# Performance work log

Hardware: AMD Instinct MI355X
Metric: run time of the kernel (lower is better)

The kernel has to match this reference:

```python
import jax, jax.numpy as jnp
import numpy as np

D = 128        # dim
S = 64         # seq_len
NSYM = 128     # symbols
STACK = 16     # stack_size
DEPTH = 8      # max_depth (ACT recursion)
THRESH = 0.99  # act_threshold
EPS = 1e-6
RES = 0.1      # residual_weight
LAM_E = 0.01   # lambda_energy
TEMP = 1.0
B = 512


def _clin(xr, xi, Wr, Wi):
    # ComplexLinear: (Wr + i Wi)(xr + i xi)
    return xr @ Wr.T - xi @ Wi.T, xr @ Wi.T + xi @ Wr.T


def _cattn(zr, zi, wr, wi):
    # ComplexAttention: complex QKV projections, real softmax over concat(real,imag)
    qr, qi = _clin(zr, zi, wr[0], wi[0])
    kr, ki = _clin(zr, zi, wr[1], wi[1])
    vr, vi = _clin(zr, zi, wr[2], wi[2])
    qf = jnp.concatenate([qr, qi], -1)
    kf = jnp.concatenate([kr, ki], -1)
    a = jax.nn.softmax(jnp.einsum('bsd,btd->bst', qf, kf) * (D ** -0.5), axis=-1)
    return jnp.einsum('bst,btd->bsd', a, vr), jnp.einsum('bst,btd->bsd', a, vi)


def setup_inputs() -> dict:
    key = jax.random.key(0)
    ks = jax.random.split(key, 12)
    sc = 1.0 / np.sqrt(D)
    return {
        'z_real': jax.random.normal(ks[0], (B, S, D), jnp.float32),
        'z_imag': jax.random.normal(ks[1], (B, S, D), jnp.float32),
        'attn_wr': jax.random.normal(ks[2], (3, D, D), jnp.float32) * sc,
        'attn_wi': jax.random.normal(ks[3], (3, D, D), jnp.float32) * sc,
        'mem_wr': jax.random.normal(ks[4], (3, D, D), jnp.float32) * sc,
        'mem_wi': jax.random.normal(ks[5], (3, D, D), jnp.float32) * sc,
        'ctrl_w': jax.random.normal(ks[6], (2 * D, 3), jnp.float32) * sc,
        'ctrl_b': jnp.zeros((3,), jnp.float32),
        'halt_w': jax.random.normal(ks[7], (2 * D, 1), jnp.float32) * sc,
        'halt_b': jnp.zeros((1,), jnp.float32),
        'codebook': jax.random.normal(ks[8], (NSYM, 2 * D), jnp.float32) * 0.2,
        'adjacency': jax.random.normal(ks[9], (NSYM, NSYM), jnp.float32),
    }


def reference(z_real, z_imag, attn_wr, attn_wi, mem_wr, mem_wi,
              ctrl_w, ctrl_b, halt_w, halt_b, codebook, adjacency):
    b = z_real.shape[0]
    mem0 = jnp.zeros((b, STACK, 2 * D), z_real.dtype)
    ptr0 = jnp.zeros((b, STACK), z_real.dtype).at[:, 0].set(1.0)
    probs0 = jnp.zeros((b, NSYM), z_real.dtype)
    halt0 = jnp.zeros((b,), z_real.dtype)
    acc0 = jnp.zeros((b, S, 2 * D), z_real.dtype)

    def step(carry, t):
        zr, zi, mem, ptr, prev_probs, halt_acc, acc = carry
        # --- complex self-attention with residual recursion ---
        ar, ai = _cattn(zr, zi, attn_wr, attn_wi)
        zr = ar + RES * zr
        zi = ai + RES * zi
        # --- memory stack (push/pop/stay pointer machine) ---
        zf = jnp.concatenate([zr.mean(1), zi.mean(1)], -1)  # [B, 2D]
        g = jax.nn.sigmoid(zf @ ctrl_w + ctrl_b)
        tot = g.sum(-1, keepdims=True) + EPS
        push, pop, stay = g[:, 0:1] / tot, g[:, 1:2] / tot, g[:, 2:3] / tot
        ptr = push * jnp.roll(ptr, 1, axis=1) + pop * jnp.roll(ptr, -1, axis=1) + stay * ptr
        mem = mem * (1 - push[..., None]) + push[..., None] * zf[:, None, :]
        amr, ami = _cattn(mem[..., :D], mem[..., D:], mem_wr, mem_wi)
        read = (jnp.concatenate([amr, ami], -1) * ptr[..., None]).sum(1)  # [B, 2D]
        zr = zr + RES * read[:, None, :D]
        zi = zi + RES * read[:, None, D:]
        # --- grounded graph VQ: codebook distance + adjacency energy bias ---
        zf = jnp.concatenate([zr.mean(1), zi.mean(1)], -1)
        d = ((zf ** 2).sum(-1, keepdims=True) + (codebook ** 2).sum(-1)
             - 2 * zf @ codebook.T) / (2 * D)
        mag = jnp.sqrt(zr ** 2 + zi ** 2)
        up = jax.nn.softplus(mag.var() / (1.0 + EPS))  # complexity modulation
        gb = prev_probs @ adjacency
        d_tot = jnp.where(t == 0, d, d - LAM_E * up * jax.nn.sigmoid(gb))
        probs = jax.nn.softmax(-d_tot / TEMP, axis=-1)
        quant = probs @ codebook
        zr = zr + RES * quant[:, None, :D]
        zi = zi + RES * quant[:, None, D:]
        # --- ACT halting accumulation ---
        p = jax.nn.sigmoid(zf @ halt_w + halt_b)[:, 0]
        running = (halt_acc < THRESH).astype(zr.dtype)
        w = jnp.where(halt_acc + p * running >= THRESH, 1.0 - halt_acc, p) * running
        halt_acc = halt_acc + w
        acc = acc + w[:, None, None] * jnp.concatenate([zr, zi], -1)
        return (zr, zi, mem, ptr, probs, halt_acc, acc), None

    carry, _ = jax.lax.scan(step, (z_real, z_imag, mem0, ptr0, probs0, halt0, acc0),
                            jnp.arange(DEPTH))
    return carry[6]  # ACT-weighted state, [B, S, 2D]
```

## Files before the change

kernel.cpp:

```cpp
#include <hip/hip_runtime.h>
#include <math.h>

#define BB 512
#define SS 64
#define DD 128
#define FF 256
#define NSYM 128
#define STK 16
#define NDEPTH 8

typedef _Float16 half_t;
typedef __attribute__((ext_vector_type(4))) _Float16 half4;
typedef __attribute__((ext_vector_type(8))) _Float16 half8;
typedef __attribute__((ext_vector_type(4))) float f32x4;

#define Z_OFF      0ull
#define QKV_OFF    8388608ull
#define WVM_OFF    33554432ull
#define MV_OFF     35651584ull
#define SIG_OFF    35782656ull
#define ZF1_OFF    41951232ull
#define ZF2_OFF    42082304ull
#define READ_OFF   42213376ull
#define PROBS_OFF  42344448ull
#define DELTA_OFF  42409984ull
#define HALT_OFF   42541056ull
#define PVAL_OFF   42541568ull
#define WACT_OFF   42542080ull
#define MAGP_OFF   42542592ull
#define CB2_OFF    42936832ull

__global__ void k_buildwt32(const float* __restrict__ wr, const float* __restrict__ wi,
                            float* __restrict__ WT32) {
    int idx = blockIdx.x * 256 + threadIdx.x;
    if (idx >= 768 * 256) return;
    int col = idx >> 8;
    int e   = idx & 255;
    int h   = col >> 8;
    int c   = col & 255;
    const float* Wr = wr + h * DD * DD;
    const float* Wi = wi + h * DD * DD;
    float v;
    if (c < DD) {
        v = (e < DD) ? Wr[c * DD + e] : -Wi[c * DD + (e - DD)];
    } else {
        int j = c - DD;
        v = (e < DD) ? Wi[j * DD + e] : Wr[j * DD + (e - DD)];
    }
    WT32[idx] = v;
}

__global__ __launch_bounds__(256) void k_buildG(const float* __restrict__ WT32,
                                                half_t* __restrict__ GTh,
                                                half_t* __restrict__ GTl) {
    __shared__ float kcol[256];
    int n = blockIdx.x;
    int e = threadIdx.x;
    kcol[e] = WT32[65536 + e * 256 + n];
    __syncthreads();
    float s = 0.f;
    for (int c = 0; c < 256; ++c) s += kcol[c] * WT32[c * 256 + e];
    half_t h = (half_t)s;
    GTh[n * 256 + e] = h;
    GTl[n * 256 + e] = (half_t)(s - (float)h);
}

__global__ void k_splitWv(const float* __restrict__ WT32,
                          half_t* __restrict__ WvTh, half_t* __restrict__ WvTl) {
    int idx = blockIdx.x * 256 + threadIdx.x;
    float v = WT32[131072 + idx];
    half_t h = (half_t)v;
    WvTh[idx] = h;
    WvTl[idx] = (half_t)(v - (float)h);
}

__global__ void k_buildWv32m(const float* __restrict__ wr, const float* __restrict__ wi,
                             float* __restrict__ Wv32m) {
    int idx = blockIdx.x * 256 + threadIdx.x;
    int e = idx >> 8;
    int c = idx & 255;
    const float* Wr = wr + 2 * DD * DD;
    const float* Wi = wi + 2 * DD * DD;
    float v;
    if (c < DD) {
        v = (e < DD) ? Wr[c * DD + e] : -Wi[c * DD + (e - DD)];
    } else {
        int j = c - DD;
        v = (e < DD) ? Wi[j * DD + e] : Wr[j * DD + (e - DD)];
    }
    Wv32m[idx] = v;
}

__global__ void k_cb2(const float* __restrict__ cb, float* __restrict__ cb2) {
    int n = threadIdx.x;
    float s = 0.f;
    for (int c = 0; c < FF; ++c) { float v = cb[n * FF + c]; s += v * v; }
    cb2[n] = s;
}

__global__ __launch_bounds__(256) void k_init(const float* __restrict__ zr_in,
                                              const float* __restrict__ zi_in,
                                              float* __restrict__ z, float* __restrict__ mv,
                                              float* __restrict__ sigma,
                                              float* __restrict__ halt, float* __restrict__ acc,
                                              float* __restrict__ delta, float* __restrict__ wact) {
    size_t idx = (size_t)blockIdx.x * 256 + threadIdx.x;
    int c = (int)(idx & 255);
    size_t bs = idx >> 8;
    z[idx] = (c < DD) ? zr_in[bs * DD + c] : zi_in[bs * DD + (c - DD)];
    acc[idx] = 0.f;
    if (idx < 131072) { mv[idx] = 0.f; delta[idx] = 0.f; }
    if (idx < 512)   { halt[idx] = 0.f; wact[idx] = 0.f; sigma[idx] = 1.f; }
}

__global__ __launch_bounds__(512, 1) void k_attn8(
        float* __restrict__ z,
        const half_t* __restrict__ GTh, const half_t* __restrict__ GTl,
        const half_t* __restrict__ WvTh, const half_t* __restrict__ WvTl,
        const float* __restrict__ delta, const float* __restrict__ wact,
        float* __restrict__ acc, float* __restrict__ zf1g) {
    __shared__ half_t Zh[16896];
    __shared__ half_t Zl[16896];
    __shared__ half_t Ubuf[2][18432];
    __shared__ half_t Pbuf[2][4][1152];
    __shared__ float Smx[4][2][16];
    __shared__ float Ssum[4][2][16];

    int b = blockIdx.x, tid = threadIdx.x;
    int w = tid >> 6, lane = tid & 63;
    int l15 = lane & 15, lq = lane >> 4;
    float* zb = z + (size_t)b * (SS * FF);
    float* accb = acc + (size_t)b * (SS * FF);

    float wa = wact[b];
    f32x4 dv = *(const f32x4*)(delta + b * FF + lane * 4);
    bool doacc = (wa != 0.0f);
#pragma unroll
    for (int it = 0; it < 8; ++it) {
        int i = w * 8 + it;
        f32x4 zv = *(const f32x4*)(zb + (size_t)i * FF + lane * 4);
        f32x4 x0;
#pragma unroll
        for (int jj = 0; jj < 4; ++jj) x0[jj] = zv[jj] + 0.1f * dv[jj];
        if (doacc) {
            f32x4 av = *(const f32x4*)(accb + (size_t)i * FF + lane * 4);
#pragma unroll
            for (int jj = 0; jj < 4; ++jj) av[jj] += wa * x0[jj];
            *(f32x4*)(accb + (size_t)i * FF + lane * 4) = av;
        }
        half4 h4, l4;
#pragma unroll
        for (int jj = 0; jj < 4; ++jj) {
            half_t h = (half_t)x0[jj];
            h4[jj] = h; l4[jj] = (half_t)(x0[jj] - (float)h);
        }
        *(half4*)&Zh[i * 264 + lane * 4] = h4;
        *(half4*)&Zl[i * 264 + lane * 4] = l4;
    }
    __syncthreads();

    {
        f32x4 tac[4][2];
#pragma unroll
        for (int mt = 0; mt < 4; ++mt)
#pragma unroll
            for (int nt = 0; nt < 2; ++nt) tac[mt][nt] = (f32x4){0.f, 0.f, 0.f, 0.f};
        __builtin_amdgcn_s_setprio(1);
#pragma unroll 2
        for (int kt = 0; kt < 8; ++kt) {
            int kc = kt * 32 + lq * 8;
            half8 ah[4], al[4], gh[2], gl[2];
#pragma unroll
            for (int mt = 0; mt < 4; ++mt) {
                int ro = (mt * 16 + l15) * 264 + kc;
                ah[mt] = *(const half8*)&Zh[ro];
                al[mt] = *(const half8*)&Zl[ro];
            }
#pragma unroll
            for (int nt = 0; nt < 2; ++nt) {
                size_t go = (size_t)(w * 32 + nt * 16 + l15) * 256 + kc;
                gh[nt] = *(const half8*)(GTh + go);
                gl[nt] = *(const half8*)(GTl + go);
            }
#pragma unroll
            for (int mt = 0; mt < 4; ++mt)
#pragma unroll
                for (int nt = 0; nt < 2; ++nt) {
                    tac[mt][nt] = __builtin_amdgcn_mfma_f32_16x16x32_f16(ah[mt], gh[nt], tac[mt][nt], 0, 0, 0);
                    tac[mt][nt] = __builtin_amdgcn_mfma_f32_16x16x32_f16(ah[mt], gl[nt], tac[mt][nt], 0, 0, 0);
                    tac[mt][nt] = __builtin_amdgcn_mfma_f32_16x16x32_f16(al[mt], gh[nt], tac[mt][nt], 0, 0, 0);
                }
        }
        __builtin_amdgcn_s_setprio(0);
        const float scale = 0.08838834764831845f;
#pragma unroll
        for (int mt = 0; mt < 4; ++mt)
#pragma unroll
            for (int nt = 0; nt < 2; ++nt)
#pragma unroll
                for (int r = 0; r < 4; ++r) {
                    int m = mt * 16 + lq * 4 + r;
                    int n = w * 32 + nt * 16 + l15;
                    float v = tac[mt][nt][r] * scale;
                    half_t h = (half_t)v;
                    Ubuf[0][m * 264 + n] = h;
                    Ubuf[1][m * 264 + n] = (half_t)(v - (float)h);
                }
    }
    __syncthreads();

    int qb = w & 3;
    int jh = w >> 2;
    float sv[2][4];
    {
        f32x4 sac[2];
        sac[0] = (f32x4){0.f, 0.f, 0.f, 0.f};
        sac[1] = (f32x4){0.f, 0.f, 0.f, 0.f};
        __builtin_amdgcn_s_setprio(1);
#pragma unroll 2
        for (int kt = 0; kt < 8; ++kt) {
            int kc = kt * 32 + lq * 8;
            int to = (qb * 16 + l15) * 264 + kc;
            half8 bh = *(const half8*)&Ubuf[0][to];
            half8 bl = *(const half8*)&Ubuf[1][to];
            half8 ah[2], al[2];
#pragma unroll
            for (int jt = 0; jt < 2; ++jt) {
                int ro = ((jh * 2 + jt) * 16 + l15) * 264 + kc;
                ah[jt] = *(const half8*)&Zh[ro];
                al[jt] = *(const half8*)&Zl[ro];
            }
#pragma unroll
            for (int jt = 0; jt < 2; ++jt) {
                sac[jt] = __builtin_amdgcn_mfma_f32_16x16x32_f16(ah[jt], bh, sac[jt], 0, 0, 0);
                sac[jt] = __builtin_amdgcn_mfma_f32_16x16x32_f16(ah[jt], bl, sac[jt], 0, 0, 0);
                sac[jt] = __builtin_amdgcn_mfma_f32_16x16x32_f16(al[jt], bh, sac[jt], 0, 0, 0);
            }
        }
        __builtin_amdgcn_s_setprio(0);
        float mxh = -1e30f;
#pragma unroll
        for (int jt = 0; jt < 2; ++jt)
#pragma unroll
            for (int r = 0; r < 4; ++r) { sv[jt][r] = sac[jt][r]; mxh = fmaxf(mxh, sv[jt][r]); }
        mxh = fmaxf(mxh, __shfl_xor(mxh, 16));
        mxh = fmaxf(mxh, __shfl_xor(mxh, 32));
        float sumh = 0.f;
#pragma unroll
        for (int jt = 0; jt < 2; ++jt)
#pragma unroll
            for (int r = 0; r < 4; ++r) { float e = expf(sv[jt][r] - mxh); sv[jt][r] = e; sumh += e; }
        sumh += __shfl_xor(sumh, 16);
        sumh += __shfl_xor(sumh, 32);
        if (lq == 0) { Smx[qb][jh][l15] = mxh; Ssum[qb][jh][l15] = sumh; }
    }

    f32x4 vac[4][2];
#pragma unroll
    for (int mt = 0; mt < 4; ++mt)
#pragma unroll
        for (int nt = 0; nt < 2; ++nt) vac[mt][nt] = (f32x4){0.f, 0.f, 0.f, 0.f};
    __builtin_amdgcn_s_setprio(1);
#pragma unroll 2
    for (int kt = 0; kt < 8; ++kt) {
        int kc = kt * 32 + lq * 8;
        half8 ah[4], al[4], gh[2], gl[2];
#pragma unroll
        for (int mt = 0; mt < 4; ++mt) {
            int ro = (mt * 16 + l15) * 264 + kc;
            ah[mt] = *(const half8*)&Zh[ro];
            al[mt] = *(const half8*)&Zl[ro];
        }
#pragma unroll
        for (int nt = 0; nt < 2; ++nt) {
            size_t go = (size_t)(w * 32 + nt * 16 + l15) * 256 + kc;
            gh[nt] = *(const half8*)(WvTh + go);
            gl[nt] = *(const half8*)(WvTl + go);
        }
#pragma unroll
        for (int mt = 0; mt < 4; ++mt)
#pragma unroll
            for (int nt = 0; nt < 2; ++nt) {
                vac[mt][nt] = __builtin_amdgcn_mfma_f32_16x16x32_f16(ah[mt], gh[nt], vac[mt][nt], 0, 0, 0);
                vac[mt][nt] = __builtin_amdgcn_mfma_f32_16x16x32_f16(ah[mt], gl[nt], vac[mt][nt], 0, 0, 0);
                vac[mt][nt] = __builtin_amdgcn_mfma_f32_16x16x32_f16(al[mt], gh[nt], vac[mt][nt], 0, 0, 0);
            }
    }
    __builtin_amdgcn_s_setprio(0);
    __syncthreads();

    {
        float mx0 = Smx[qb][0][l15], mx1 = Smx[qb][1][l15];
        float gmx = fmaxf(mx0, mx1);
        float ssum = Ssum[qb][0][l15] * expf(mx0 - gmx) + Ssum[qb][1][l15] * expf(mx1 - gmx);
        float pscale = expf(((jh == 0) ? mx0 : mx1) - gmx) / ssum;
#pragma unroll
        for (int jt = 0; jt < 2; ++jt) {
            half4 h4, l4;
#pragma unroll
            for (int r = 0; r < 4; ++r) {
                float pv = sv[jt][r] * pscale;
                half_t hh = (half_t)pv;
                h4[r] = hh;
                l4[r] = (half_t)(pv - (float)hh);
            }
            int po = l15 * 72 + (jh * 2 + jt) * 16 + lq * 4;
            *(half4*)&Pbuf[0][qb][po] = h4;
            *(half4*)&Pbuf[1][qb][po] = l4;
        }
    }

#pragma unroll
    for (int mt = 0; mt < 4; ++mt)
#pragma unroll
        for (int nt = 0; nt < 2; ++nt) {
            int n = w * 32 + nt * 16 + l15;
            int m0 = mt * 16 + lq * 4;
            half4 h4, l4;
#pragma unroll
            for (int r = 0; r < 4; ++r) {
                float v = vac[mt][nt][r];
                half_t h = (half_t)v;
                h4[r] = h; l4[r] = (half_t)(v - (float)h);
            }
            *(half4*)&Ubuf[0][n * 72 + m0] = h4;
            *(half4*)&Ubuf[1][n * 72 + m0] = l4;
        }
    __syncthreads();

    f32x4 oc[4][2];
#pragma unroll
    for (int mt = 0; mt < 4; ++mt)
#pragma unroll
        for (int nt = 0; nt < 2; ++nt) oc[mt][nt] = (f32x4){0.f, 0.f, 0.f, 0.f};
    __builtin_amdgcn_s_setprio(1);
#pragma unroll
    for (int kt = 0; kt < 2; ++kt) {
        half8 pah[4], pal[4];
#pragma unroll
        for (int mt = 0; mt < 4; ++mt) {
            int po = l15 * 72 + kt * 32 + lq * 8;
            pah[mt] = *(const half8*)&Pbuf[0][mt][po];
            pal[mt] = *(const half8*)&Pbuf[1][mt][po];
        }
#pragma unroll
        for (int nt = 0; nt < 2; ++nt) {
            int n = w * 32 + nt * 16 + l15;
            half8 vbh = *(const half8*)&Ubuf[0][n * 72 + kt * 32 + lq * 8];
            half8 vbl = *(const half8*)&Ubuf[1][n * 72 + kt * 32 + lq * 8];
#pragma unroll
            for (int mt = 0; mt < 4; ++mt) {
                oc[mt][nt] = __builtin_amdgcn_mfma_f32_16x16x32_f16(pah[mt], vbh, oc[mt][nt], 0, 0, 0);
                oc[mt][nt] = __builtin_amdgcn_mfma_f32_16x16x32_f16(pah[mt], vbl, oc[mt][nt], 0, 0, 0);
                oc[mt][nt] = __builtin_amdgcn_mfma_f32_16x16x32_f16(pal[mt], vbh, oc[mt][nt], 0, 0, 0);
            }
        }
    }
    __builtin_amdgcn_s_setprio(0);

    float zfs[2] = {0.f, 0.f};
#pragma unroll
    for (int mt = 0; mt < 4; ++mt)
#pragma unroll
        for (int nt = 0; nt < 2; ++nt)
#pragma unroll
            for (int r = 0; r < 4; ++r) {
                int i = mt * 16 + lq * 4 + r;
                int c = w * 32 + nt * 16 + l15;
                int zo = i * 264 + c;
                float x0 = (float)Zh[zo] + (float)Zl[zo];
                float z1 = oc[mt][nt][r] + 0.1f * x0;
                zb[(size_t)i * FF + c] = z1;
                zfs[nt] += z1;
            }
#pragma unroll
    for (int nt = 0; nt < 2; ++nt) {
        zfs[nt] += __shfl_xor(zfs[nt], 16);
        zfs[nt] += __shfl_xor(zfs[nt], 32);
    }
    if (lq == 0) {
#pragma unroll
        for (int nt = 0; nt < 2; ++nt)
            zf1g[b * FF + w * 32 + nt * 16 + l15] = zfs[nt] * (1.f / 64.f);
    }
}

__global__ __launch_bounds__(256) void k_stack3(
        const float* __restrict__ zf1,
        const float* __restrict__ ctrl_w, const float* __restrict__ ctrl_b,
        float* __restrict__ sigma, float* __restrict__ mv,
        const float* __restrict__ Wv32m,
        float* __restrict__ readv, float* __restrict__ zf2,
        const float* __restrict__ halt_w, const float* __restrict__ halt_b,
        float* __restrict__ pval,
        const float* __restrict__ z, float* __restrict__ magpart) {
    __shared__ float zf[256];
    __shared__ float g[3];
    __shared__ float rd[256];
    __shared__ float red[256];

    int b = blockIdx.x, tid = threadIdx.x;
    int w = tid >> 6, lane = tid & 63;

    zf[tid] = zf1[b * FF + tid];
    __syncthreads();

    float zw = 0.f;
#pragma unroll 8
    for (int e = 0; e < 256; ++e) zw += Wv32m[e * 256 + tid] * zf[e];

    if (w < 3) {
        float s = 0.f;
#pragma unroll
        for (int q = 0; q < 4; ++q) {
            int c = lane + 64 * q;
            s += zf[c] * ctrl_w[c * 3 + w];
        }
#pragma unroll
        for (int off = 1; off < 64; off <<= 1) s += __shfl_xor(s, off);
        if (lane == 0) g[w] = 1.f / (1.f + expf(-(s + ctrl_b[w])));
    }
    __syncthreads();
    float tot = g[0] + g[1] + g[2] + 1e-6f;
    float push = g[0] / tot, pop = g[1] / tot, stay = g[2] / tot;
    float signew = sigma[b] * (push + pop + stay);
    if (tid == 0) sigma[b] = signew;

    float omp = 1.f - push;
    float m2v = mv[b * FF + tid] * omp + push * zw;
    mv[b * FF + tid] = m2v;

    float a = signew * m2v;
    rd[tid] = a;
    readv[b * FF + tid] = a;
    float z2 = zf[tid] + 0.1f * a;
    zf2[b * FF + tid] = z2;
    red[tid] = z2 * halt_w[tid];
    __syncthreads();
    for (int off = 128; off > 0; off >>= 1) {
        if (tid < off) red[tid] += red[tid + off];
        __syncthreads();
    }
    if (tid == 0) pval[b] = 1.f / (1.f + expf(-(red[0] + halt_b[0])));
    __syncthreads();

    {
        int d = tid & 127, hf = tid >> 7;
        float rr = 0.1f * rd[d];
        float ri = 0.1f * rd[DD + d];
        const float* zb = z + (size_t)b * (SS * FF);
        float ms = 0.f, msq = 0.f;
        for (int s32 = 0; s32 < 32; ++s32) {
            int s = hf * 32 + s32;
            float zr = zb[s * FF + d] + rr;
            float zi = zb[s * FF + DD + d] + ri;
            float m2 = zr * zr + zi * zi;
            ms += sqrtf(m2); msq += m2;
        }
        red[tid] = ms;
        __syncthreads();
        for (int off = 128; off > 0; off >>= 1) {
            if (tid < off) red[tid] += red[tid + off];
            __syncthreads();
        }
        float tms = red[0];
        __syncthreads();
        red[tid] = msq;
        __syncthreads();
        for (int off = 128; off > 0; off >>= 1) {
            if (tid < off) red[tid] += red[tid + off];
            __syncthreads();
        }
        if (tid == 0) { magpart[2 * b] = tms; magpart[2 * b + 1] = red[0]; }
    }
}

__global__ __launch_bounds__(256) void k_vq2(
        const float* __restrict__ zf2g, const float* __restrict__ readv,
        float* __restrict__ probs, float* __restrict__ halt,
        const float* __restrict__ pvalg, const float* __restrict__ magp,
        const float* __restrict__ cb, const float* __restrict__ cb2,
        const float* __restrict__ adj,
        float* __restrict__ delta, float* __restrict__ wact,
        const float* __restrict__ z, float* __restrict__ acc,
        int t, int last) {
    __shared__ float zf[256];
    __shared__ float pr[128];
    __shared__ float upred[8];
    __shared__ float zzred[4];
    __shared__ float mxred[4];
    __shared__ float sered[4];
    __shared__ float waS[1];

    int b = blockIdx.x, tid = threadIdx.x;
    int w = tid >> 6, lane = tid & 63;

    zf[tid] = zf2g[b * FF + tid];

    float up = 0.f;
    if (t > 0) {
        f32x4 mv4 = *(const f32x4*)(magp + tid * 4);
        float pa = mv4[0] + mv4[2];
        float pb = mv4[1] + mv4[3];
#pragma unroll
        for (int off = 1; off < 64; off <<= 1) {
            pa += __shfl_xor(pa, off);
            pb += __shfl_xor(pb, off);
        }
        if (lane == 0) { upred[w * 2] = pa; upred[w * 2 + 1] = pb; }
    }
    __syncthreads();
    if (t > 0) {
        float tms  = upred[0] + upred[2] + upred[4] + upred[6];
        float tmsq = upred[1] + upred[3] + upred[5] + upred[7];
        const float N = 4194304.f;
        float mean = tms / N;
        float var = tmsq / N - mean * mean;
        float x = var / (1.f + 1e-6f);
        up = (x > 20.f) ? x : log1pf(expf(x));
    }

    {
        float part = zf[tid] * zf[tid];
#pragma unroll
        for (int off = 1; off < 64; off <<= 1) part += __shfl_xor(part, off);
        if (lane == 0) zzred[w] = part;
    }
    __syncthreads();
    float zz = zzred[0] + zzred[1] + zzred[2] + zzred[3];

    int n = tid >> 1, half = tid & 1;
    float dacc = 0.f;
    {
        const float* cbn = cb + n * FF + half * 128;
        const float* zfp = zf + half * 128;
#pragma unroll 8
        for (int c2 = 0; c2 < 128; c2 += 4) {
            f32x4 cv = *(const f32x4*)(cbn + c2);
            dacc += cv[0] * zfp[c2] + cv[1] * zfp[c2 + 1] + cv[2] * zfp[c2 + 2] + cv[3] * zfp[c2 + 3];
        }
        dacc += __shfl_xor(dacc, 1);
    }
    float gacc = 0.f;
    if (t > 0) {
        const float* pp = probs + b * NSYM;
        for (int k = half * 64; k < half * 64 + 64; ++k)
            gacc += pp[k] * adj[k * NSYM + n];
        gacc += __shfl_xor(gacc, 1);
    }

    float dist = (zz + cb2[n] - 2.f * dacc) * (1.f / 256.f);
    float dtot = dist;
    if (t > 0) dtot = dist - 0.01f * up * (1.f / (1.f + expf(-gacc)));
    float vval = -dtot;

    {
        float m = vval;
#pragma unroll
        for (int off = 1; off < 64; off <<= 1) m = fmaxf(m, __shfl_xor(m, off));
        if (lane == 0) mxred[w] = m;
    }
    __syncthreads();
    float mx = fmaxf(fmaxf(mxred[0], mxred[1]), fmaxf(mxred[2], mxred[3]));

    float e = expf(vval - mx);
    {
        float s = (half == 0) ? e : 0.f;
#pragma unroll
        for (int off = 1; off < 64; off <<= 1) s += __shfl_xor(s, off);
        if (lane == 0) sered[w] = s;
    }
    __syncthreads();
    float se = sered[0] + sered[1] + sered[2] + sered[3];
    float psm = e / se;
    if (half == 0) {
        pr[n] = psm;
        probs[b * NSYM + n] = psm;
    }
    __syncthreads();

    float q = 0.f;
#pragma unroll 4
    for (int k = 0; k < NSYM; ++k) q += pr[k] * cb[k * FF + tid];
    float dltc = readv[b * FF + tid] + q;
    delta[b * FF + tid] = dltc;

    if (tid == 0) {
        float h = halt[b], p = pvalg[b];
        float running = (h < 0.99f) ? 1.f : 0.f;
        float w2 = (((h + p * running) >= 0.99f) ? (1.f - h) : p) * running;
        halt[b] = h + w2;
        wact[b] = w2;
        waS[0] = w2;
    }

    if (last) {
        __syncthreads();
        float wa = waS[0];
        if (wa != 0.0f) {
            const float* zb = z + (size_t)b * (SS * FF);
            float* ab = acc + (size_t)b * (SS * FF);
            for (int s = 0; s < SS; ++s)
                ab[s * FF + tid] += wa * (zb[s * FF + tid] + 0.1f * dltc);
        }
    }
}

extern "C" void kernel_launch(void* const* d_in, const int* in_sizes, int n_in,
                              void* d_out, int out_size, void* d_ws, size_t ws_size,
                              hipStream_t stream) {
    const float* z_real  = (const float*)d_in[0];
    const float* z_imag  = (const float*)d_in[1];
    const float* attn_wr = (const float*)d_in[2];
    const float* attn_wi = (const float*)d_in[3];
    const float* mem_wr  = (const float*)d_in[4];
    const float* mem_wi  = (const float*)d_in[5];
    const float* ctrl_w  = (const float*)d_in[6];
    const float* ctrl_b  = (const float*)d_in[7];
    const float* halt_w  = (const float*)d_in[8];
    const float* halt_b  = (const float*)d_in[9];
    const float* codebook  = (const float*)d_in[10];
    const float* adjacency = (const float*)d_in[11];

    float* ws = (float*)d_ws;
    float* z      = ws + Z_OFF;
    float* WT32   = ws + QKV_OFF;
    half_t* GTh   = (half_t*)(ws + QKV_OFF + 196608);
    half_t* GTl   = GTh + 65536;
    half_t* WvTh  = GTl + 65536;
    half_t* WvTl  = WvTh + 65536;
    float* Wv32m  = ws + WVM_OFF;
    float* mv     = ws + MV_OFF;
    float* sigma  = ws + SIG_OFF;
    float* zf1    = ws + ZF1_OFF;
    float* zf2    = ws + ZF2_OFF;
    float* readv  = ws + READ_OFF;
    float* probs  = ws + PROBS_OFF;
    float* delta  = ws + DELTA_OFF;
    float* halt   = ws + HALT_OFF;
    float* pval   = ws + PVAL_OFF;
    float* wact   = ws + WACT_OFF;
    float* magp   = ws + MAGP_OFF;
    float* cb2    = ws + CB2_OFF;
    float* acc    = (float*)d_out;

    k_buildwt32<<<768, 256, 0, stream>>>(attn_wr, attn_wi, WT32);
    k_buildG<<<256, 256, 0, stream>>>(WT32, GTh, GTl);
    k_splitWv<<<256, 256, 0, stream>>>(WT32, WvTh, WvTl);
    k_buildWv32m<<<256, 256, 0, stream>>>(mem_wr, mem_wi, Wv32m);
    k_cb2<<<1, 128, 0, stream>>>(codebook, cb2);
    k_init<<<32768, 256, 0, stream>>>(z_real, z_imag, z, mv, sigma, halt, acc,
                                      delta, wact);

    for (int t = 0; t < NDEPTH; ++t) {
        k_attn8<<<BB, 512, 0, stream>>>(z, GTh, GTl, WvTh, WvTl, delta, wact, acc, zf1);
        k_stack3<<<BB, 256, 0, stream>>>(zf1, ctrl_w, ctrl_b, sigma, mv, Wv32m,
                                         readv, zf2, halt_w, halt_b, pval, z, magp);
        k_vq2<<<BB, 256, 0, stream>>>(zf2, readv, probs, halt, pval, magp,
                                      codebook, cb2, adjacency, delta, wact,
                                      z, acc, t, (t == NDEPTH - 1) ? 1 : 0);
    }
}
```

Measured before the change: 781.7 us.

## Fuse stack-memory update and magnitude statistics into attention kernel

Merges the k_stack3 kernel into k_attn8 so the per-batch mean vector, stack controller, memory-read, halting logit and magnitude partial sums are computed in the same block that produced z. The new z tile is kept in shared memory (reusing the Zh/Zl region as fp32) so the magnitude pass reads from LDS instead of re-reading z from global memory. Tree reductions are replaced with wave shuffles. This removes one kernel launch per depth step and a global round trip of z, at the cost of a larger shared-memory footprint and more work per attention block.

```diff
diff --git a/kernel.cpp b/kernel.cpp
--- a/kernel.cpp
+++ b/kernel.cpp
@@ -19,7 +19,6 @@
 #define WVM_OFF    33554432ull
 #define MV_OFF     35651584ull
 #define SIG_OFF    35782656ull
-#define ZF1_OFF    41951232ull
 #define ZF2_OFF    42082304ull
 #define READ_OFF   42213376ull
 #define PROBS_OFF  42344448ull
@@ -118,19 +117,35 @@
         const half_t* __restrict__ GTh, const half_t* __restrict__ GTl,
         const half_t* __restrict__ WvTh, const half_t* __restrict__ WvTl,
         const float* __restrict__ delta, const float* __restrict__ wact,
-        float* __restrict__ acc, float* __restrict__ zf1g) {
-    __shared__ half_t Zh[16896];
-    __shared__ half_t Zl[16896];
-    __shared__ half_t Ubuf[2][18432];
-    __shared__ half_t Pbuf[2][4][1152];
-    __shared__ float Smx[4][2][16];
-    __shared__ float Ssum[4][2][16];
+        float* __restrict__ acc,
+        const float* __restrict__ Wv32m,
+        const float* __restrict__ ctrl_w, const float* __restrict__ ctrl_b,
+        const float* __restrict__ halt_w, const float* __restrict__ halt_b,
+        float* __restrict__ sigma, float* __restrict__ mv,
+        float* __restrict__ readv, float* __restrict__ zf2,
+        float* __restrict__ pval, float* __restrict__ magpart) {
+    __shared__ __align__(16) char smem[160768];
+    half_t* Zh = (half_t*)smem;
+    half_t* Zl = (half_t*)(smem + 33792);
+    float*  Zf = (float*)smem;
+    half_t* U0 = (half_t*)(smem + 67584);
+    half_t* U1 = (half_t*)(smem + 104448);
+    half_t* P0 = (half_t*)(smem + 141312);
+    half_t* P1 = (half_t*)(smem + 150528);
+    float* Smx = (float*)(smem + 159744);
+    float* Ssu = (float*)(smem + 160256);
+    float* zfS = (float*)(smem + 67584);
+    float* zwS = (float*)(smem + 68608);
+    float* rdS = (float*)(smem + 69632);
+    float* redS= (float*)(smem + 70656);
+    float* gS  = (float*)(smem + 71680);
 
     int b = blockIdx.x, tid = threadIdx.x;
     int w = tid >> 6, lane = tid & 63;
     int l15 = lane & 15, lq = lane >> 4;
     float* zb = z + (size_t)b * (SS * FF);
     float* accb = acc + (size_t)b * (SS * FF);
+    float sigold = sigma[b];
 
     float wa = wact[b];
     f32x4 dv = *(const f32x4*)(delta + b * FF + lane * 4);
@@ -203,8 +218,8 @@
                     int n = w * 32 + nt * 16 + l15;
                     float v = tac[mt][nt][r] * scale;
                     half_t h = (half_t)v;
-                    Ubuf[0][m * 264 + n] = h;
-                    Ubuf[1][m * 264 + n] = (half_t)(v - (float)h);
+                    U0[m * 264 + n] = h;
+                    U1[m * 264 + n] = (half_t)(v - (float)h);
                 }
     }
     __syncthreads();
@@ -221,8 +236,8 @@
         for (int kt = 0; kt < 8; ++kt) {
             int kc = kt * 32 + lq * 8;
             int to = (qb * 16 + l15) * 264 + kc;
-            half8 bh = *(const half8*)&Ubuf[0][to];
-            half8 bl = *(const half8*)&Ubuf[1][to];
+            half8 bh = *(const half8*)&U0[to];
+            half8 bl = *(const half8*)&U1[to];
             half8 ah[2], al[2];
 #pragma unroll
             for (int jt = 0; jt < 2; ++jt) {
@@ -252,7 +267,7 @@
             for (int r = 0; r < 4; ++r) { float e = expf(sv[jt][r] - mxh); sv[jt][r] = e; sumh += e; }
         sumh += __shfl_xor(sumh, 16);
         sumh += __shfl_xor(sumh, 32);
-        if (lq == 0) { Smx[qb][jh][l15] = mxh; Ssum[qb][jh][l15] = sumh; }
+        if (lq == 0) { Smx[(qb * 2 + jh) * 16 + l15] = mxh; Ssu[(qb * 2 + jh) * 16 + l15] = sumh; }
     }
 
     f32x4 vac[4][2];
@@ -290,9 +305,10 @@
     __syncthreads();
 
     {
-        float mx0 = Smx[qb][0][l15], mx1 = Smx[qb][1][l15];
+        float mx0 = Smx[(qb * 2 + 0) * 16 + l15], mx1 = Smx[(qb * 2 + 1) * 16 + l15];
         float gmx = fmaxf(mx0, mx1);
-        float ssum = Ssum[qb][0][l15] * expf(mx0 - gmx) + Ssum[qb][1][l15] * expf(mx1 - gmx);
+        float ssum = Ssu[(qb * 2 + 0) * 16 + l15] * expf(mx0 - gmx)
+                   + Ssu[(qb * 2 + 1) * 16 + l15] * expf(mx1 - gmx);
         float pscale = expf(((jh == 0) ? mx0 : mx1) - gmx) / ssum;
 #pragma unroll
         for (int jt = 0; jt < 2; ++jt) {
@@ -305,8 +321,8 @@
                 l4[r] = (half_t)(pv - (float)hh);
             }
             int po = l15 * 72 + (jh * 2 + jt) * 16 + lq * 4;
-            *(half4*)&Pbuf[0][qb][po] = h4;
-            *(half4*)&Pbuf[1][qb][po] = l4;
+            *(half4*)&P0[qb * 1152 + po] = h4;
+            *(half4*)&P1[qb * 1152 + po] = l4;
         }
     }
 
@@ -323,8 +339,8 @@
                 half_t h = (half_t)v;
                 h4[r] = h; l4[r] = (half_t)(v - (float)h);
             }
-            *(half4*)&Ubuf[0][n * 72 + m0] = h4;
-            *(half4*)&Ubuf[1][n * 72 + m0] = l4;
+            *(half4*)&U0[n * 72 + m0] = h4;
+            *(half4*)&U1[n * 72 + m0] = l4;
         }
     __syncthreads();
 
@@ -340,14 +356,14 @@
 #pragma unroll
         for (int mt = 0; mt < 4; ++mt) {
             int po = l15 * 72 + kt * 32 + lq * 8;
-            pah[mt] = *(const half8*)&Pbuf[0][mt][po];
-            pal[mt] = *(const half8*)&Pbuf[1][mt][po];
+            pah[mt] = *(const half8*)&P0[mt * 1152 + po];
+            pal[mt] = *(const half8*)&P1[mt * 1152 + po];
         }
 #pragma unroll
         for (int nt = 0; nt < 2; ++nt) {
             int n = w * 32 + nt * 16 + l15;
-            half8 vbh = *(const half8*)&Ubuf[0][n * 72 + kt * 32 + lq * 8];
-            half8 vbl = *(const half8*)&Ubuf[1][n * 72 + kt * 32 + lq * 8];
+            half8 vbh = *(const half8*)&U0[n * 72 + kt * 32 + lq * 8];
+            half8 vbl = *(const half8*)&U1[n * 72 + kt * 32 + lq * 8];
 #pragma unroll
             for (int mt = 0; mt < 4; ++mt) {
                 oc[mt][nt] = __builtin_amdgcn_mfma_f32_16x16x32_f16(pah[mt], vbh, oc[mt][nt], 0, 0, 0);
@@ -370,6 +386,7 @@
                 int zo = i * 264 + c;
                 float x0 = (float)Zh[zo] + (float)Zl[zo];
                 float z1 = oc[mt][nt][r] + 0.1f * x0;
+                oc[mt][nt][r] = z1;
                 zb[(size_t)i * FF + c] = z1;
                 zfs[nt] += z1;
             }
@@ -378,100 +395,98 @@
         zfs[nt] += __shfl_xor(zfs[nt], 16);
         zfs[nt] += __shfl_xor(zfs[nt], 32);
     }
+    __syncthreads();
+
+#pragma unroll
+    for (int mt = 0; mt < 4; ++mt)
+#pragma unroll
+        for (int nt = 0; nt < 2; ++nt)
+#pragma unroll
+            for (int r = 0; r < 4; ++r) {
+                int i = mt * 16 + lq * 4 + r;
+                int c = w * 32 + nt * 16 + l15;
+                Zf[i * 256 + c] = oc[mt][nt][r];
+            }
     if (lq == 0) {
 #pragma unroll
         for (int nt = 0; nt < 2; ++nt)
-            zf1g[b * FF + w * 32 + nt * 16 + l15] = zfs[nt] * (1.f / 64.f);
-    }
-}
-
-__global__ __launch_bounds__(256) void k_stack3(
-        const float* __restrict__ zf1,
-        const float* __restrict__ ctrl_w, const float* __restrict__ ctrl_b,
-        float* __restrict__ sigma, float* __restrict__ mv,
-        const float* __restrict__ Wv32m,
-        float* __restrict__ readv, float* __restrict__ zf2,
-        const float* __restrict__ halt_w, const float* __restrict__ halt_b,
-        float* __restrict__ pval,
-        const float* __restrict__ z, float* __restrict__ magpart) {
-    __shared__ float zf[256];
-    __shared__ float g[3];
-    __shared__ float rd[256];
-    __shared__ float red[256];
-
-    int b = blockIdx.x, tid = threadIdx.x;
-    int w = tid >> 6, lane = tid & 63;
-
-    zf[tid] = zf1[b * FF + tid];
-    __syncthreads();
-
-    float zw = 0.f;
-#pragma unroll 8
-    for (int e = 0; e < 256; ++e) zw += Wv32m[e * 256 + tid] * zf[e];
+            zfS[w * 32 + nt * 16 + l15] = zfs[nt] * (1.f / 64.f);
+    }
+    __syncthreads();
 
     if (w < 3) {
         float s = 0.f;
 #pragma unroll
         for (int q = 0; q < 4; ++q) {
             int c = lane + 64 * q;
-            s += zf[c] * ctrl_w[c * 3 + w];
+            s += zfS[c] * ctrl_w[c * 3 + w];
         }
 #pragma unroll
         for (int off = 1; off < 64; off <<= 1) s += __shfl_xor(s, off);
-        if (lane == 0) g[w] = 1.f / (1.f + expf(-(s + ctrl_b[w])));
-    }
-    __syncthreads();
-    float tot = g[0] + g[1] + g[2] + 1e-6f;
-    float push = g[0] / tot, pop = g[1] / tot, stay = g[2] / tot;
-    float signew = sigma[b] * (push + pop + stay);
-    if (tid == 0) sigma[b] = signew;
-
-    float omp = 1.f - push;
-    float m2v = mv[b * FF + tid] * omp + push * zw;
-    mv[b * FF + tid] = m2v;
-
-    float a = signew * m2v;
-    rd[tid] = a;
-    readv[b * FF + tid] = a;
-    float z2 = zf[tid] + 0.1f * a;
-    zf2[b * FF + tid] = z2;
-    red[tid] = z2 * halt_w[tid];
-    __syncthreads();
-    for (int off = 128; off > 0; off >>= 1) {
-        if (tid < off) red[tid] += red[tid + off];
-        __syncthreads();
-    }
-    if (tid == 0) pval[b] = 1.f / (1.f + expf(-(red[0] + halt_b[0])));
-    __syncthreads();
-
-    {
-        int d = tid & 127, hf = tid >> 7;
-        float rr = 0.1f * rd[d];
-        float ri = 0.1f * rd[DD + d];
-        const float* zb = z + (size_t)b * (SS * FF);
+        if (lane == 0) gS[w] = 1.f / (1.f + expf(-(s + ctrl_b[w])));
+    } else if (w >= 4) {
+        int c = (w - 4) * 64 + lane;
+        float s = 0.f;
+#pragma unroll 8
+        for (int e = 0; e < 256; ++e) s += Wv32m[e * 256 + c] * zfS[e];
+        zwS[c] = s;
+    }
+    __syncthreads();
+
+    float z2 = 0.f;
+    {
+        float tot = gS[0] + gS[1] + gS[2] + 1e-6f;
+        float push = gS[0] / tot, pop = gS[1] / tot, stay = gS[2] / tot;
+        float signew = sigold * (push + pop + stay);
+        if (tid == 0) sigma[b] = signew;
+        if (tid < 256) {
+            float m2v = mv[b * FF + tid] * (1.f - push) + push * zwS[tid];
+            mv[b * FF + tid] = m2v;
+            float a = signew * m2v;
+            rdS[tid] = a;
+            readv[b * FF + tid] = a;
+            z2 = zfS[tid] + 0.1f * a;
+            zf2[b * FF + tid] = z2;
+        }
+    }
+    {
+        float hp = (tid < 256) ? z2 * halt_w[tid] : 0.f;
+#pragma unroll
+        for (int off = 1; off < 64; off <<= 1) hp += __shfl_xor(hp, off);
+        if (lane == 0) redS[w] = hp;
+    }
+    __syncthreads();
+    if (tid == 0) {
+        float s = redS[0] + redS[1] + redS[2] + redS[3] + redS[4] + redS[5] + redS[6] + redS[7];
+        pval[b] = 1.f / (1.f + expf(-(s + halt_b[0])));
+    }
+
+    {
+        int d = tid & 127, seg = tid >> 7;
+        float rr = 0.1f * rdS[d];
+        float ri = 0.1f * rdS[DD + d];
         float ms = 0.f, msq = 0.f;
-        for (int s32 = 0; s32 < 32; ++s32) {
-            int s = hf * 32 + s32;
-            float zr = zb[s * FF + d] + rr;
-            float zi = zb[s * FF + DD + d] + ri;
+#pragma unroll 4
+        for (int r16 = 0; r16 < 16; ++r16) {
+            int s = seg * 16 + r16;
+            float zr = Zf[s * 256 + d] + rr;
+            float zi = Zf[s * 256 + DD + d] + ri;
             float m2 = zr * zr + zi * zi;
             ms += sqrtf(m2); msq += m2;
         }
-        red[tid] = ms;
-        __syncthreads();
-        for (int off = 128; off > 0; off >>= 1) {
-            if (tid < off) red[tid] += red[tid + off];
-            __syncthreads();
-        }
-        float tms = red[0];
-        __syncthreads();
-        red[tid] = msq;
-        __syncthreads();
-        for (int off = 128; off > 0; off >>= 1) {
-            if (tid < off) red[tid] += red[tid + off];
-            __syncthreads();
-        }
-        if (tid == 0) { magpart[2 * b] = tms; magpart[2 * b + 1] = red[0]; }
+#pragma unroll
+        for (int off = 1; off < 64; off <<= 1) {
+            ms  += __shfl_xor(ms, off);
+            msq += __shfl_xor(msq, off);
+        }
+        if (lane == 0) { redS[8 + w] = ms; redS[16 + w] = msq; }
+    }
+    __syncthreads();
+    if (tid == 0) {
+        float tms  = redS[8]  + redS[9]  + redS[10] + redS[11] + redS[12] + redS[13] + redS[14] + redS[15];
+        float tmsq = redS[16] + redS[17] + redS[18] + redS[19] + redS[20] + redS[21] + redS[22] + redS[23];
+        magpart[2 * b] = tms;
+        magpart[2 * b + 1] = tmsq;
     }
 }
 
@@ -632,7 +647,6 @@
     float* Wv32m  = ws + WVM_OFF;
     float* mv     = ws + MV_OFF;
     float* sigma  = ws + SIG_OFF;
-    float* zf1    = ws + ZF1_OFF;
     float* zf2    = ws + ZF2_OFF;
     float* readv  = ws + READ_OFF;
     float* probs  = ws + PROBS_OFF;
@@ -653,9 +667,9 @@
                                       delta, wact);
 
     for (int t = 0; t < NDEPTH; ++t) {
-        k_attn8<<<BB, 512, 0, stream>>>(z, GTh, GTl, WvTh, WvTl, delta, wact, acc, zf1);
-        k_stack3<<<BB, 256, 0, stream>>>(zf1, ctrl_w, ctrl_b, sigma, mv, Wv32m,
-                                         readv, zf2, halt_w, halt_b, pval, z, magp);
+        k_attn8<<<BB, 512, 0, stream>>>(z, GTh, GTl, WvTh, WvTl, delta, wact, acc,
+                                        Wv32m, ctrl_w, ctrl_b, halt_w, halt_b,
+                                        sigma, mv, readv, zf2, pval, magp);
         k_vq2<<<BB, 256, 0, stream>>>(zf2, readv, probs, halt, pval, magp,
                                       codebook, cb2, adjacency, delta, wact,
                                       z, acc, t, (t == NDEPTH - 1) ? 1 : 0);
```

After: 800.6 us. 2.4% more time.
